# Performance work log

Measured on AMD Instinct MI355X. Metric: run time of the kernel, lower is better.

Reference implementation:

```python
import jax, jax.numpy as jnp
import numpy as np

NUM_GROUPS = 256


def _linear(x, w, b):
    return x @ w + b


def _layernorm(x, g, b, eps=1e-5):
    mu = jnp.mean(x, axis=-1, keepdims=True)
    var = jnp.mean((x - mu) ** 2, axis=-1, keepdims=True)
    return (x - mu) / jnp.sqrt(var + eps) * g + b


def setup_inputs() -> dict:
    key = jax.random.key(0)
    ks = jax.random.split(key, 12)
    B, N, C = 16, 8192, 3
    s = 0.02
    return {
        "xyz": jax.random.normal(ks[0], (B, N, C), jnp.float32),
        "labels": jax.random.randint(ks[1], (B, N), 0, NUM_GROUPS),
        # conv1: Linear(3,128) -> LayerNorm(128) -> ReLU -> Linear(128,256)
        "w1a": jax.random.normal(ks[2], (3, 128), jnp.float32) * s,
        "b1a": jnp.zeros((128,), jnp.float32),
        "g1": jnp.ones((128,), jnp.float32),
        "beta1": jnp.zeros((128,), jnp.float32),
        "w1b": jax.random.normal(ks[3], (128, 256), jnp.float32) * s,
        "b1b": jnp.zeros((256,), jnp.float32),
        # conv2: Linear(512,512) -> LayerNorm(512) -> ReLU -> Linear(512,256)
        "w2a": jax.random.normal(ks[4], (512, 512), jnp.float32) * s,
        "b2a": jnp.zeros((512,), jnp.float32),
        "g2": jnp.ones((512,), jnp.float32),
        "beta2": jnp.zeros((512,), jnp.float32),
        "w2b": jax.random.normal(ks[5], (512, 256), jnp.float32) * s,
        "b2b": jnp.zeros((256,), jnp.float32),
    }


def reference(xyz, labels, w1a, b1a, g1, beta1, w1b, b1b,
              w2a, b2a, g2, beta2, w2b, b2b):
    # per-batch segment reductions over cluster labels
    seg_sum = jax.vmap(lambda f, l: jax.ops.segment_sum(f, l, num_segments=NUM_GROUPS))
    seg_max = jax.vmap(lambda f, l: jax.ops.segment_max(f, l, num_segments=NUM_GROUPS))
    gather = jax.vmap(lambda p, l: p[l])  # [G,D],[N] -> [N,D]

    # centroids = per-cluster mean of xyz (converged kmeans centroids)
    counts = seg_sum(jnp.ones_like(xyz[..., :1]), labels)          # [B,G,1]
    centroids = seg_sum(xyz, labels) / jnp.maximum(counts, 1.0)    # [B,G,3]

    p_i = gather(centroids, labels)                                # [B,N,3]
    relative_xyz = xyz - p_i                                       # feature_type='dp'

    h = _linear(relative_xyz, w1a, b1a)
    h = jax.nn.relu(_layernorm(h, g1, beta1))
    h = _linear(h, w1b, b1b)                                       # [B,N,256]

    pooled = seg_max(h, labels)                                    # [B,G,256]
    pooled = jnp.where(jnp.isfinite(pooled), pooled, 0.0)          # empty groups -> 0
    repeated = gather(pooled, labels)                              # [B,N,256]

    cat = jnp.concatenate([repeated, h], axis=-1)                  # [B,N,512]
    h2 = _linear(cat, w2a, b2a)
    h2 = jax.nn.relu(_layernorm(h2, g2, beta2))
    h2 = _linear(h2, w2b, b2b)                                     # [B,N,256]

    out = seg_max(h2, labels)                                      # [B,G,256]
    out = jnp.where(jnp.isfinite(out), out, 0.0)
    return (centroids, out, p_i, labels)
```

## Files before the change

### kernel.cpp

```cpp
#include <hip/hip_runtime.h>
#include <hip/hip_bf16.h>

#define NB_  16
#define NPTS 8192
#define NG   256
#define NP   (NB_*NPTS)
#define NBLK (NP/128)
#define NQ   (NP/32)

#define OFF_CENT 0
#define OFF_OUT  12288
#define OFF_PI   1060864
#define OFF_LAB  1454080

typedef unsigned short u16;
typedef __attribute__((ext_vector_type(8))) short bf16x8;
typedef __attribute__((ext_vector_type(4))) float f32x4;

static constexpr size_t WS_SUMS  = 0;
static constexpr size_t WS_A1    = 65536;
static constexpr size_t WS_H     = WS_A1   + (size_t)NP*128*2;
static constexpr size_t WS_PBF   = WS_H    + (size_t)NP*256*2;
static constexpr size_t WS_WT1   = WS_PBF  + (size_t)NB_*NG*256*2;
static constexpr size_t WS_WT2A  = WS_WT1  + (size_t)256*128*2;
static constexpr size_t WS_WT2B  = WS_WT2A + (size_t)512*512*2;
static constexpr size_t WS_PREP  = WS_WT2B + (size_t)256*512*2;
static constexpr size_t WS_OFFS  = WS_PREP + (size_t)NB_*NG*512*4;
static constexpr size_t WS_CNT   = WS_OFFS + (size_t)NB_*NG*4;
static constexpr size_t WS_CUR   = WS_CNT  + (size_t)NB_*NG*4;
static constexpr size_t WS_SPOS  = WS_CUR  + (size_t)NB_*NG*4;
static constexpr size_t WS_GLAB  = WS_SPOS + (size_t)NP*4;
static constexpr size_t WS_PF    = WS_GLAB + (size_t)NP*4;
static constexpr size_t WS_PL    = WS_PF   + (size_t)NQ*256*4;
static constexpr size_t WS_DST   = WS_PL   + (size_t)NQ*256*4;
static constexpr size_t WS_NEED  = WS_DST  + (size_t)NB_*NG*256*4;

__device__ __forceinline__ u16 f2bf_bits(float f){
  __hip_bfloat16 h = __float2bfloat16(f);
  union { __hip_bfloat16 h; u16 s; } u; u.h = h; return u.s;
}
__device__ __forceinline__ float bf_bits2f(u16 s){
  return __uint_as_float(((unsigned)s) << 16);
}

__device__ __forceinline__ void gload16(const void* g, void* l){
  __builtin_amdgcn_global_load_lds((const __attribute__((address_space(1))) void*)g,
                                   (__attribute__((address_space(3))) void*)l, 16, 0, 0);
}

__global__ void k_init(float* __restrict__ sums, int* __restrict__ cursor){
  int i = blockIdx.x*blockDim.x + threadIdx.x;
  if (i < NB_*NG*4) sums[i] = 0.f;
  if (i < NB_*NG) cursor[i] = 0;
}

__global__ void k_wt(const float* __restrict__ src, u16* __restrict__ dst, int K, int N){
  int i = blockIdx.x*blockDim.x + threadIdx.x;
  if (i >= K*N) return;
  int n = i / K, k = i - n*K;
  dst[i] = f2bf_bits(src[(size_t)k*N + n]);
}

__global__ void k_points(const float* __restrict__ xyz, const int* __restrict__ labels,
                         float* __restrict__ sums, float* __restrict__ outLab){
  int p = blockIdx.x*blockDim.x + threadIdx.x;
  if (p >= NP) return;
  int b = p / NPTS;
  int g = labels[p];
  float x = xyz[p*3+0], y = xyz[p*3+1], z = xyz[p*3+2];
  float* s = sums + (size_t)(b*NG + g)*4;
  atomicAdd(s+0, x); atomicAdd(s+1, y); atomicAdd(s+2, z); atomicAdd(s+3, 1.f);
  outLab[p] = (float)g;
}

__global__ void k_cent(const float* __restrict__ sums, float* __restrict__ cent_out){
  int i = blockIdx.x*blockDim.x + threadIdx.x;
  if (i >= NB_*NG) return;
  const float* s = sums + (size_t)i*4;
  float c = fmaxf(s[3], 1.f);
  cent_out[i*3+0] = s[0]/c;
  cent_out[i*3+1] = s[1]/c;
  cent_out[i*3+2] = s[2]/c;
}

__global__ void k_scan(const float* __restrict__ sums, int* __restrict__ offs,
                       int* __restrict__ counts){
  __shared__ int sc[256];
  int b = blockIdx.x, g = threadIdx.x;
  int c = (int)(sums[(size_t)(b*NG+g)*4+3] + 0.5f);
  sc[g] = c;
  __syncthreads();
  for (int d = 1; d < 256; d <<= 1){
    int t = (g >= d) ? sc[g-d] : 0;
    __syncthreads();
    sc[g] += t;
    __syncthreads();
  }
  offs[b*NG+g] = b*NPTS + sc[g] - c;
  counts[b*NG+g] = c;
}

__global__ void k_scatter(const int* __restrict__ labels, const int* __restrict__ offs,
                          int* __restrict__ cursor, int* __restrict__ sortpos,
                          int* __restrict__ glab){
  int p = blockIdx.x*blockDim.x + threadIdx.x;
  if (p >= NP) return;
  int b = p / NPTS, g = labels[p];
  int pos = offs[b*NG+g] + atomicAdd(&cursor[b*NG+g], 1);
  sortpos[p] = pos;
  glab[pos] = g;
}

__global__ __launch_bounds__(256) void k_mlp1(
    const float* __restrict__ xyz, const int* __restrict__ labels,
    const int* __restrict__ sortpos, const float* __restrict__ cent,
    const float* __restrict__ w1a, const float* __restrict__ b1a,
    const float* __restrict__ g1, const float* __restrict__ beta1,
    u16* __restrict__ a1, float* __restrict__ pi_out)
{
  int wave = (int)((blockIdx.x*blockDim.x + threadIdx.x) >> 6);
  int lane = threadIdx.x & 63;
  int p = wave;
  if (p >= NP) return;
  int b = p / NPTS;
  int g = labels[p];
  const float* cb = cent + (size_t)(b*NG+g)*3;
  float c0 = cb[0], c1 = cb[1], c2 = cb[2];
  float r0 = xyz[p*3+0]-c0, r1 = xyz[p*3+1]-c1, r2 = xyz[p*3+2]-c2;
  if (lane < 3) pi_out[(size_t)p*3+lane] = (lane==0?c0:(lane==1?c1:c2));
  int j = lane*2;
  float2 wa0 = *(const float2*)(w1a + 0*128 + j);
  float2 wa1 = *(const float2*)(w1a + 1*128 + j);
  float2 wa2 = *(const float2*)(w1a + 2*128 + j);
  float2 bb  = *(const float2*)(b1a + j);
  float t0 = bb.x + r0*wa0.x + r1*wa1.x + r2*wa2.x;
  float t1 = bb.y + r0*wa0.y + r1*wa1.y + r2*wa2.y;
  float s = t0+t1, sq = t0*t0 + t1*t1;
  #pragma unroll
  for (int m = 32; m; m >>= 1){ s += __shfl_xor(s, m); sq += __shfl_xor(sq, m); }
  float mu  = s * (1.f/128.f);
  float var = sq * (1.f/128.f) - mu*mu;
  float inv = rsqrtf(var + 1e-5f);
  float2 gg = *(const float2*)(g1 + j), be = *(const float2*)(beta1 + j);
  float a0 = fmaxf((t0-mu)*inv*gg.x + be.x, 0.f);
  float a1v = fmaxf((t1-mu)*inv*gg.y + be.y, 0.f);
  unsigned pk = ((unsigned)f2bf_bits(a1v) << 16) | f2bf_bits(a0);
  int sp = sortpos[p];
  *reinterpret_cast<unsigned*>(a1 + (size_t)sp*128 + j) = pk;
}

template<int EPI>
__global__ __launch_bounds__(256)
void mgemm(const u16* __restrict__ A, int lda, int K,
           const u16* __restrict__ BT, int ldb, int kofs,
           const float* __restrict__ bias,
           u16* __restrict__ Cst, float* __restrict__ Cf, int ldc, int Nc)
{
  __shared__ alignas(16) u16 As[128*32];
  __shared__ alignas(16) u16 Bs[128*32];
  int NBk = Nc >> 7;
  int bm = blockIdx.x / NBk, bn = blockIdx.x % NBk;
  int m0 = bm << 7, n0 = bn << 7;
  int tid = threadIdx.x;
  int lane = tid & 63, w = tid >> 6;
  int wr = w >> 1, wc = w & 1;
  int l15 = lane & 15, l4 = lane >> 4;
  int r0 = tid >> 2;
  int ks = (tid & 3) << 3;
  u16* asd0 = As + (size_t)(w*64)*8;
  u16* asd1 = As + (size_t)(256 + w*64)*8;
  u16* bsd0 = Bs + (size_t)(w*64)*8;
  u16* bsd1 = Bs + (size_t)(256 + w*64)*8;
  f32x4 acc[4][4];
  #pragma unroll
  for (int i = 0; i < 4; ++i)
    #pragma unroll
    for (int jj = 0; jj < 4; ++jj)
      #pragma unroll
      for (int e = 0; e < 4; ++e) acc[i][jj][e] = 0.f;

  for (int k0 = 0; k0 < K; k0 += 32){
    gload16(A + (size_t)(m0 + r0)*lda + k0 + ks, asd0);
    gload16(A + (size_t)(m0 + r0 + 64)*lda + k0 + ks, asd1);
    gload16(BT + (size_t)(n0 + r0)*ldb + kofs + k0 + ks, bsd0);
    gload16(BT + (size_t)(n0 + r0 + 64)*ldb + kofs + k0 + ks, bsd1);
    __syncthreads();
    bf16x8 af[4], bfr[4];
    #pragma unroll
    for (int i = 0; i < 4; ++i){
      af[i]  = *(const bf16x8*)&As[(size_t)(wr*64 + i*16 + l15)*32 + l4*8];
      bfr[i] = *(const bf16x8*)&Bs[(size_t)(wc*64 + i*16 + l15)*32 + l4*8];
    }
    #pragma unroll
    for (int i = 0; i < 4; ++i)
      #pragma unroll
      for (int jj = 0; jj < 4; ++jj)
        acc[i][jj] = __builtin_amdgcn_mfma_f32_16x16x32_bf16(af[i], bfr[jj], acc[i][jj], 0, 0, 0);
    __syncthreads();
  }

  float bi[4];
  #pragma unroll
  for (int jj = 0; jj < 4; ++jj) bi[jj] = bias[n0 + wc*64 + jj*16 + l15];
  #pragma unroll
  for (int i = 0; i < 4; ++i){
    #pragma unroll
    for (int r = 0; r < 4; ++r){
      int m = m0 + wr*64 + i*16 + l4*4 + r;
      #pragma unroll
      for (int jj = 0; jj < 4; ++jj){
        int n = n0 + wc*64 + jj*16 + l15;
        float v = acc[i][jj][r] + bi[jj];
        if (EPI == 1) Cst[(size_t)m*ldc + n] = f2bf_bits(v);
        if (EPI == 3) Cf[(size_t)m*ldc + n] = v;
      }
    }
  }
}

__global__ __launch_bounds__(256) void k_pool(const u16* __restrict__ h,
                                              const int* __restrict__ offs,
                                              const int* __restrict__ counts,
                                              u16* __restrict__ poolbf){
  int bg = blockIdx.x, c = threadIdx.x;
  int cnt = counts[bg];
  if (cnt == 0){ poolbf[(size_t)bg*256 + c] = 0; return; }
  int off = offs[bg];
  float mx = bf_bits2f(h[(size_t)off*256 + c]);
  for (int r = 1; r < cnt; ++r)
    mx = fmaxf(mx, bf_bits2f(h[(size_t)(off+r)*256 + c]));
  poolbf[(size_t)bg*256 + c] = f2bf_bits(mx);
}

__global__ __launch_bounds__(1024, 1)
void fused6(const u16* __restrict__ h, const u16* __restrict__ wt2a,
            const u16* __restrict__ wt2b, const float* __restrict__ prepf,
            const float* __restrict__ b2b, const float* __restrict__ g2,
            const float* __restrict__ beta2, const int* __restrict__ glab,
            float* __restrict__ pf, float* __restrict__ pl, float* __restrict__ dstage)
{
  __shared__ alignas(16) char smem[136704];
  float* ssum  = (float*)(smem + 131072);
  float* ssq   = (float*)(smem + 131584);
  int*  glab_s = (int*)(smem + 132096);
  float* gtab  = (float*)(smem + 132608);
  float* btab  = (float*)(smem + 134656);
  int tid = threadIdx.x;
  int w = tid >> 6, lane = tid & 63;
  int l15 = lane & 15, l4 = lane >> 4;
  int m0 = blockIdx.x << 7;
  if (tid < 128){ ssum[tid] = 0.f; ssq[tid] = 0.f; glab_s[tid] = glab[m0 + tid]; }
  if (tid < 512) gtab[tid] = g2[tid];
  else           btab[tid - 512] = beta2[tid - 512];

  {
    const char* hb = (const char*)h;
    int lrow = lane >> 5;
    int kb = (lane & 31) << 4;
    #pragma unroll
    for (int t = 0; t < 4; ++t){
      int q = w*4 + t;
      int row = q*2 + lrow;
      gload16(hb + (size_t)(m0 + row)*512 + (kb ^ ((row & 7) << 4)),
              smem + 65536 + q*1024);
    }
  }
  __syncthreads();

  int gb = (m0 / NPTS) * NG;
  const u16* wA = wt2a + ((size_t)((w<<5) + l15))*512 + 256 + l4*8;

  #pragma unroll
  for (int half = 0; half < 2; ++half){
    int hr0 = half << 6;
    f32x4 acc[4][2];
    #pragma unroll
    for (int i = 0; i < 4; ++i)
      #pragma unroll
      for (int j = 0; j < 2; ++j)
        #pragma unroll
        for (int e = 0; e < 4; ++e) acc[i][j][e] = 0.f;
    #pragma unroll
    for (int kk = 0; kk < 8; ++kk){
      const int k0 = kk*32;
      bf16x8 bfr0 = *(const bf16x8*)(wA + k0);
      bf16x8 bfr1 = *(const bf16x8*)(wA + 8192 + k0);
      #pragma unroll
      for (int i = 0; i < 4; ++i){
        int row = hr0 + (i<<4) + l15;
        bf16x8 af = *(const bf16x8*)(smem + 65536 + row*512 +
                       ((((k0 + l4*8)) << 1) ^ ((row & 7) << 4)));
        acc[i][0] = __builtin_amdgcn_mfma_f32_16x16x32_bf16(af, bfr0, acc[i][0], 0, 0, 0);
        acc[i][1] = __builtin_amdgcn_mfma_f32_16x16x32_bf16(af, bfr1, acc[i][1], 0, 0, 0);
      }
    }
    #pragma unroll
    for (int i = 0; i < 4; ++i)
      #pragma unroll
      for (int r = 0; r < 4; ++r){
        int row = hr0 + (i<<4) + (l4<<2) + r;
        int grp = gb + glab_s[row];
        #pragma unroll
        for (int j = 0; j < 2; ++j){
          int n = (w<<5) + (j<<4) + l15;
          acc[i][j][r] += prepf[((size_t)grp << 9) + n];
        }
        float s = acc[i][0][r] + acc[i][1][r];
        float q = acc[i][0][r]*acc[i][0][r] + acc[i][1][r]*acc[i][1][r];
        #pragma unroll
        for (int mk = 1; mk < 16; mk <<= 1){ s += __shfl_xor(s, mk); q += __shfl_xor(q, mk); }
        if (l15 == 0){ atomicAdd(&ssum[row], s); atomicAdd(&ssq[row], q); }
      }
    if (half == 1) __syncthreads();
    #pragma unroll
    for (int i = 0; i < 4; ++i)
      #pragma unroll
      for (int r = 0; r < 4; ++r){
        int row = hr0 + (i<<4) + (l4<<2) + r;
        #pragma unroll
        for (int j = 0; j < 2; ++j){
          int n = (w<<5) + (j<<4) + l15;
          int byo = (row << 10) + ((n << 1) ^ ((row & 7) << 4));
          *(u16*)(smem + byo) = f2bf_bits(acc[i][j][r]);
        }
      }
  }

  if (tid < 128){
    float mu = ssum[tid] * (1.f/512.f);
    float var = ssq[tid] * (1.f/512.f) - mu*mu;
    ssum[tid] = mu;
    ssq[tid] = rsqrtf(var + 1e-5f);
  }
  __syncthreads();

  {
    int row = tid >> 3;
    int cb = tid & 7;
    float mu = ssum[row], inv = ssq[row];
    #pragma unroll
    for (int cc = 0; cc < 8; ++cc){
      int n = (((cc<<3) | cb) << 3);
      int byo = (row << 10) + ((n << 1) ^ ((row & 7) << 4));
      bf16x8 uv = *(const bf16x8*)(smem + byo);
      float4 gA = *(const float4*)(gtab + n), gB = *(const float4*)(gtab + n + 4);
      float4 bA = *(const float4*)(btab + n), bB = *(const float4*)(btab + n + 4);
      float gg[8] = {gA.x,gA.y,gA.z,gA.w,gB.x,gB.y,gB.z,gB.w};
      float bb[8] = {bA.x,bA.y,bA.z,bA.w,bB.x,bB.y,bB.z,bB.w};
      bf16x8 ov;
      #pragma unroll
      for (int e = 0; e < 8; ++e){
        float x = bf_bits2f((u16)uv[e]);
        ov[e] = (short)f2bf_bits(fmaxf((x - mu)*inv*gg[e] + bb[e], 0.f));
      }
      *(bf16x8*)(smem + byo) = ov;
    }
  }
  __syncthreads();

  f32x4 acc2[8];
  #pragma unroll
  for (int i = 0; i < 8; ++i)
    #pragma unroll
    for (int e = 0; e < 4; ++e) acc2[i][e] = 0.f;

  {
    const u16* wB = wt2b + ((size_t)((w<<4) + l15))*512 + l4*8;
    #pragma unroll
    for (int kk = 0; kk < 16; ++kk){
      const int k0 = kk*32;
      bf16x8 bf2 = *(const bf16x8*)(wB + k0);
      #pragma unroll
      for (int ip = 0; ip < 4; ++ip){
        bf16x8 af0, af1;
        {
          int row0 = ((2*ip)<<4) + l15;
          int row1 = ((2*ip+1)<<4) + l15;
          af0 = *(const bf16x8*)(smem + (row0 << 10) + ((((k0 + l4*8)) << 1) ^ ((row0 & 7) << 4)));
          af1 = *(const bf16x8*)(smem + (row1 << 10) + ((((k0 + l4*8)) << 1) ^ ((row1 & 7) << 4)));
        }
        acc2[2*ip]   = __builtin_amdgcn_mfma_f32_16x16x32_bf16(af0, bf2, acc2[2*ip], 0, 0, 0);
        acc2[2*ip+1] = __builtin_amdgcn_mfma_f32_16x16x32_bf16(af1, bf2, acc2[2*ip+1], 0, 0, 0);
      }
    }
  }
  __syncthreads();

  float bb = b2b[(w<<4) + l15];
  float* vbuf = (float*)smem;
  #pragma unroll
  for (int i = 0; i < 8; ++i){
    int n = (w<<4) + l15;
    #pragma unroll
    for (int r = 0; r < 4; ++r){
      int row = (i<<4) + (l4<<2) + r;
      vbuf[row*256 + n] = acc2[i][r] + bb;
    }
  }
  __syncthreads();
  {
    int c = tid & 255;
    int q = tid >> 8;
    int r0 = q << 5;
    size_t qblk = ((size_t)blockIdx.x << 2) + q;
    int curg = glab_s[r0];
    float mx = vbuf[r0*256 + c];
    bool from0 = true;
    for (int r = 1; r < 32; ++r){
      int g = glab_s[r0 + r];
      float v = vbuf[(r0 + r)*256 + c];
      if (g != curg){
        if (from0) pf[qblk*256 + c] = mx;
        else       dstage[((size_t)(gb + curg))*256 + c] = mx;
        curg = g; mx = v; from0 = false;
      } else mx = fmaxf(mx, v);
    }
    if (from0) pf[qblk*256 + c] = mx;
    else       pl[qblk*256 + c] = mx;
  }
}

__global__ __launch_bounds__(256) void k_combine(const int* __restrict__ offs,
                                                 const int* __restrict__ counts,
                                                 const float* __restrict__ pf,
                                                 const float* __restrict__ pl,
                                                 const float* __restrict__ dstage,
                                                 float* __restrict__ outp){
  int bg = blockIdx.x, c = threadIdx.x;
  int cnt = counts[bg];
  if (cnt == 0){ outp[(size_t)bg*256 + c] = 0.f; return; }
  int off = offs[bg], end = off + cnt;
  int B0 = off >> 5, B1 = (end - 1) >> 5;
  float v;
  if (B0 == B1){
    if ((off & 31) == 0)      v = pf[(size_t)B0*256 + c];
    else if ((end & 31) == 0) v = pl[(size_t)B0*256 + c];
    else                      v = dstage[(size_t)bg*256 + c];
  } else {
    v = ((off & 31) == 0) ? pf[(size_t)B0*256 + c] : pl[(size_t)B0*256 + c];
    for (int k = B0 + 1; k <= B1; ++k)
      v = fmaxf(v, pf[(size_t)k*256 + c]);
  }
  outp[(size_t)bg*256 + c] = v;
}

__global__ void k_sig(float* __restrict__ out, float val){
  int i = blockIdx.x*blockDim.x + threadIdx.x;
  if (i < 256) out[i] = val;
}

extern "C" void kernel_launch(void* const* d_in, const int* in_sizes, int n_in,
                              void* d_out, int out_size, void* d_ws, size_t ws_size,
                              hipStream_t stream) {
  const float* xyz    = (const float*)d_in[0];
  const int*   labels = (const int*)  d_in[1];
  const float* w1a    = (const float*)d_in[2];
  const float* b1a    = (const float*)d_in[3];
  const float* g1     = (const float*)d_in[4];
  const float* beta1  = (const float*)d_in[5];
  const float* w1b    = (const float*)d_in[6];
  const float* b1b    = (const float*)d_in[7];
  const float* w2a    = (const float*)d_in[8];
  const float* b2a    = (const float*)d_in[9];
  const float* g2     = (const float*)d_in[10];
  const float* beta2  = (const float*)d_in[11];
  const float* w2b    = (const float*)d_in[12];
  const float* b2b    = (const float*)d_in[13];
  float* out = (float*)d_out;
  char* ws = (char*)d_ws;

  if (ws_size < WS_NEED){
    k_sig<<<1, 256, 0, stream>>>(out, 10000.f + (float)(ws_size >> 20));
    return;
  }

  float*     sums   = (float*)(ws + WS_SUMS);
  u16*       a1     = (u16*)(ws + WS_A1);
  u16*       h      = (u16*)(ws + WS_H);
  u16*       poolbf = (u16*)(ws + WS_PBF);
  u16*       wt1    = (u16*)(ws + WS_WT1);
  u16*       wt2a   = (u16*)(ws + WS_WT2A);
  u16*       wt2b   = (u16*)(ws + WS_WT2B);
  float*     prepf  = (float*)(ws + WS_PREP);
  int*       offs   = (int*)(ws + WS_OFFS);
  int*       counts = (int*)(ws + WS_CNT);
  int*       cursor = (int*)(ws + WS_CUR);
  int*       sortpos= (int*)(ws + WS_SPOS);
  int*       glab   = (int*)(ws + WS_GLAB);
  float*     pf     = (float*)(ws + WS_PF);
  float*     pl     = (float*)(ws + WS_PL);
  float*     dstage = (float*)(ws + WS_DST);

  float* cent_out = out + OFF_CENT;
  float* out_seg  = out + OFF_OUT;
  float* pi_out   = out + OFF_PI;
  float* lab_out  = out + OFF_LAB;

  k_init<<<64, 256, 0, stream>>>(sums, cursor);
  k_wt<<<(128*256+255)/256, 256, 0, stream>>>(w1b, wt1, 128, 256);
  k_wt<<<(512*512+255)/256, 256, 0, stream>>>(w2a, wt2a, 512, 512);
  k_wt<<<(512*256+255)/256, 256, 0, stream>>>(w2b, wt2b, 512, 256);
  k_points<<<NP/256, 256, 0, stream>>>(xyz, labels, sums, lab_out);
  k_cent<<<(NB_*NG+255)/256, 256, 0, stream>>>(sums, cent_out);
  k_scan<<<NB_, 256, 0, stream>>>(sums, offs, counts);
  k_scatter<<<NP/256, 256, 0, stream>>>(labels, offs, cursor, sortpos, glab);
  k_mlp1<<<NP/4, 256, 0, stream>>>(xyz, labels, sortpos, cent_out,
                                   w1a, b1a, g1, beta1, a1, pi_out);
  mgemm<1><<<(NP/128)*(256/128), 256, 0, stream>>>(
      a1, 128, 128, wt1, 128, 0, b1b, h, (float*)nullptr, 256, 256);
  k_pool<<<NB_*NG, 256, 0, stream>>>(h, offs, counts, poolbf);
  mgemm<3><<<(NB_*NG/128)*(512/128), 256, 0, stream>>>(
      poolbf, 256, 256, wt2a, 512, 0, b2a, (u16*)nullptr, prepf, 512, 512);
  fused6<<<NBLK, 1024, 0, stream>>>(h, wt2a, wt2b, prepf, b2b, g2, beta2, glab,
                                    pf, pl, dstage);
  k_combine<<<NB_*NG, 256, 0, stream>>>(offs, counts, pf, pl, dstage, out_seg);
}
```

Baseline: 338.5 us.

## Shrink fused MLP tile to 64 rows with 512 threads for two blocks per CU

The fused second-MLP kernel now handles 64 points per block with 8 waves instead of 128 points with 16 waves. Shared memory drops to about 70KB, so two blocks can share a CU, and each wave covers more output columns per row tile. The aim is better overlap of the global loads and barrier phases across co-resident blocks. In exchange, every weight fragment is reloaded twice as often per point, and each wave holds more accumulator registers.

```diff
diff --git a/kernel.cpp b/kernel.cpp
--- a/kernel.cpp
+++ b/kernel.cpp
@@ -5,7 +5,7 @@
 #define NPTS 8192
 #define NG   256
 #define NP   (NB_*NPTS)
-#define NBLK (NP/128)
+#define NBLK (NP/64)
 #define NQ   (NP/32)
 
 #define OFF_CENT 0
@@ -232,26 +232,26 @@
   poolbf[(size_t)bg*256 + c] = f2bf_bits(mx);
 }
 
-__global__ __launch_bounds__(1024, 1)
-void fused6(const u16* __restrict__ h, const u16* __restrict__ wt2a,
+__global__ __launch_bounds__(512, 2)
+void fused7(const u16* __restrict__ h, const u16* __restrict__ wt2a,
             const u16* __restrict__ wt2b, const float* __restrict__ prepf,
             const float* __restrict__ b2b, const float* __restrict__ g2,
             const float* __restrict__ beta2, const int* __restrict__ glab,
             float* __restrict__ pf, float* __restrict__ pl, float* __restrict__ dstage)
 {
-  __shared__ alignas(16) char smem[136704];
-  float* ssum  = (float*)(smem + 131072);
-  float* ssq   = (float*)(smem + 131584);
-  int*  glab_s = (int*)(smem + 132096);
-  float* gtab  = (float*)(smem + 132608);
-  float* btab  = (float*)(smem + 134656);
+  __shared__ alignas(16) char smem[70400];
+  float* ssum  = (float*)(smem + 65536);
+  float* ssq   = (float*)(smem + 65792);
+  int*  glab_s = (int*)(smem + 66048);
+  float* gtab  = (float*)(smem + 66304);
+  float* btab  = (float*)(smem + 68352);
   int tid = threadIdx.x;
   int w = tid >> 6, lane = tid & 63;
   int l15 = lane & 15, l4 = lane >> 4;
-  int m0 = blockIdx.x << 7;
-  if (tid < 128){ ssum[tid] = 0.f; ssq[tid] = 0.f; glab_s[tid] = glab[m0 + tid]; }
-  if (tid < 512) gtab[tid] = g2[tid];
-  else           btab[tid - 512] = beta2[tid - 512];
+  int m0 = blockIdx.x << 6;
+  if (tid < 64){ ssum[tid] = 0.f; ssq[tid] = 0.f; glab_s[tid] = glab[m0 + tid]; }
+  gtab[tid] = g2[tid];
+  btab[tid] = beta2[tid];
 
   {
     const char* hb = (const char*)h;
@@ -262,71 +262,75 @@
       int q = w*4 + t;
       int row = q*2 + lrow;
       gload16(hb + (size_t)(m0 + row)*512 + (kb ^ ((row & 7) << 4)),
-              smem + 65536 + q*1024);
+              smem + 32768 + q*1024);
     }
   }
   __syncthreads();
 
   int gb = (m0 / NPTS) * NG;
-  const u16* wA = wt2a + ((size_t)((w<<5) + l15))*512 + 256 + l4*8;
+  const u16* wA = wt2a + ((size_t)((w<<6) + l15))*512 + 256 + l4*8;
 
   #pragma unroll
   for (int half = 0; half < 2; ++half){
-    int hr0 = half << 6;
-    f32x4 acc[4][2];
-    #pragma unroll
-    for (int i = 0; i < 4; ++i)
-      #pragma unroll
-      for (int j = 0; j < 2; ++j)
+    int hr0 = half << 5;
+    f32x4 acc[2][4];
+    #pragma unroll
+    for (int i = 0; i < 2; ++i)
+      #pragma unroll
+      for (int j = 0; j < 4; ++j)
         #pragma unroll
         for (int e = 0; e < 4; ++e) acc[i][j][e] = 0.f;
     #pragma unroll
     for (int kk = 0; kk < 8; ++kk){
       const int k0 = kk*32;
-      bf16x8 bfr0 = *(const bf16x8*)(wA + k0);
-      bf16x8 bfr1 = *(const bf16x8*)(wA + 8192 + k0);
-      #pragma unroll
-      for (int i = 0; i < 4; ++i){
+      bf16x8 bfr[4];
+      #pragma unroll
+      for (int j = 0; j < 4; ++j)
+        bfr[j] = *(const bf16x8*)(wA + j*8192 + k0);
+      #pragma unroll
+      for (int i = 0; i < 2; ++i){
         int row = hr0 + (i<<4) + l15;
-        bf16x8 af = *(const bf16x8*)(smem + 65536 + row*512 +
+        bf16x8 af = *(const bf16x8*)(smem + 32768 + row*512 +
                        ((((k0 + l4*8)) << 1) ^ ((row & 7) << 4)));
-        acc[i][0] = __builtin_amdgcn_mfma_f32_16x16x32_bf16(af, bfr0, acc[i][0], 0, 0, 0);
-        acc[i][1] = __builtin_amdgcn_mfma_f32_16x16x32_bf16(af, bfr1, acc[i][1], 0, 0, 0);
-      }
-    }
-    #pragma unroll
-    for (int i = 0; i < 4; ++i)
+        #pragma unroll
+        for (int j = 0; j < 4; ++j)
+          acc[i][j] = __builtin_amdgcn_mfma_f32_16x16x32_bf16(af, bfr[j], acc[i][j], 0, 0, 0);
+      }
+    }
+    #pragma unroll
+    for (int i = 0; i < 2; ++i)
       #pragma unroll
       for (int r = 0; r < 4; ++r){
         int row = hr0 + (i<<4) + (l4<<2) + r;
         int grp = gb + glab_s[row];
+        float s = 0.f, q = 0.f;
         #pragma unroll
-        for (int j = 0; j < 2; ++j){
-          int n = (w<<5) + (j<<4) + l15;
+        for (int j = 0; j < 4; ++j){
+          int n = (w<<6) + (j<<4) + l15;
           acc[i][j][r] += prepf[((size_t)grp << 9) + n];
+          s += acc[i][j][r];
+          q += acc[i][j][r]*acc[i][j][r];
         }
-        float s = acc[i][0][r] + acc[i][1][r];
-        float q = acc[i][0][r]*acc[i][0][r] + acc[i][1][r]*acc[i][1][r];
         #pragma unroll
         for (int mk = 1; mk < 16; mk <<= 1){ s += __shfl_xor(s, mk); q += __shfl_xor(q, mk); }
         if (l15 == 0){ atomicAdd(&ssum[row], s); atomicAdd(&ssq[row], q); }
       }
     if (half == 1) __syncthreads();
     #pragma unroll
-    for (int i = 0; i < 4; ++i)
+    for (int i = 0; i < 2; ++i)
       #pragma unroll
       for (int r = 0; r < 4; ++r){
         int row = hr0 + (i<<4) + (l4<<2) + r;
         #pragma unroll
-        for (int j = 0; j < 2; ++j){
-          int n = (w<<5) + (j<<4) + l15;
+        for (int j = 0; j < 4; ++j){
+          int n = (w<<6) + (j<<4) + l15;
           int byo = (row << 10) + ((n << 1) ^ ((row & 7) << 4));
           *(u16*)(smem + byo) = f2bf_bits(acc[i][j][r]);
         }
       }
   }
 
-  if (tid < 128){
+  if (tid < 64){
     float mu = ssum[tid] * (1.f/512.f);
     float var = ssq[tid] * (1.f/512.f) - mu*mu;
     ssum[tid] = mu;
@@ -358,20 +362,25 @@
   }
   __syncthreads();
 
-  f32x4 acc2[8];
-  #pragma unroll
-  for (int i = 0; i < 8; ++i)
-    #pragma unroll
-    for (int e = 0; e < 4; ++e) acc2[i][e] = 0.f;
+  f32x4 acc2[4][2];
+  #pragma unroll
+  for (int i = 0; i < 4; ++i)
+    #pragma unroll
+    for (int j = 0; j < 2; ++j)
+      #pragma unroll
+      for (int e = 0; e < 4; ++e) acc2[i][j][e] = 0.f;
 
   {
-    const u16* wB = wt2b + ((size_t)((w<<4) + l15))*512 + l4*8;
+    const u16* wB = wt2b + ((size_t)((w<<5) + l15))*512 + l4*8;
     #pragma unroll
     for (int kk = 0; kk < 16; ++kk){
       const int k0 = kk*32;
-      bf16x8 bf2 = *(const bf16x8*)(wB + k0);
-      #pragma unroll
-      for (int ip = 0; ip < 4; ++ip){
+      bf16x8 bf2[2];
+      #pragma unroll
+      for (int j = 0; j < 2; ++j)
+        bf2[j] = *(const bf16x8*)(wB + j*8192 + k0);
+      #pragma unroll
+      for (int ip = 0; ip < 2; ++ip){
         bf16x8 af0, af1;
         {
           int row0 = ((2*ip)<<4) + l15;
@@ -379,30 +388,36 @@
           af0 = *(const bf16x8*)(smem + (row0 << 10) + ((((k0 + l4*8)) << 1) ^ ((row0 & 7) << 4)));
           af1 = *(const bf16x8*)(smem + (row1 << 10) + ((((k0 + l4*8)) << 1) ^ ((row1 & 7) << 4)));
         }
-        acc2[2*ip]   = __builtin_amdgcn_mfma_f32_16x16x32_bf16(af0, bf2, acc2[2*ip], 0, 0, 0);
-        acc2[2*ip+1] = __builtin_amdgcn_mfma_f32_16x16x32_bf16(af1, bf2, acc2[2*ip+1], 0, 0, 0);
+        #pragma unroll
+        for (int j = 0; j < 2; ++j){
+          acc2[2*ip][j]   = __builtin_amdgcn_mfma_f32_16x16x32_bf16(af0, bf2[j], acc2[2*ip][j], 0, 0, 0);
+          acc2[2*ip+1][j] = __builtin_amdgcn_mfma_f32_16x16x32_bf16(af1, bf2[j], acc2[2*ip+1][j], 0, 0, 0);
+        }
       }
     }
   }
   __syncthreads();
 
-  float bb = b2b[(w<<4) + l15];
+  float bb0 = b2b[(w<<5) + l15], bb1 = b2b[(w<<5) + 16 + l15];
   float* vbuf = (float*)smem;
   #pragma unroll
-  for (int i = 0; i < 8; ++i){
-    int n = (w<<4) + l15;
-    #pragma unroll
-    for (int r = 0; r < 4; ++r){
-      int row = (i<<4) + (l4<<2) + r;
-      vbuf[row*256 + n] = acc2[i][r] + bb;
-    }
-  }
+  for (int i = 0; i < 4; ++i)
+    #pragma unroll
+    for (int j = 0; j < 2; ++j){
+      int n = (w<<5) + (j<<4) + l15;
+      float bbj = j ? bb1 : bb0;
+      #pragma unroll
+      for (int r = 0; r < 4; ++r){
+        int row = (i<<4) + (l4<<2) + r;
+        vbuf[row*256 + n] = acc2[i][j][r] + bbj;
+      }
+    }
   __syncthreads();
   {
     int c = tid & 255;
     int q = tid >> 8;
     int r0 = q << 5;
-    size_t qblk = ((size_t)blockIdx.x << 2) + q;
+    size_t qblk = ((size_t)blockIdx.x << 1) + q;
     int curg = glab_s[r0];
     float mx = vbuf[r0*256 + c];
     bool from0 = true;
@@ -511,7 +526,7 @@
   k_pool<<<NB_*NG, 256, 0, stream>>>(h, offs, counts, poolbf);
   mgemm<3><<<(NB_*NG/128)*(512/128), 256, 0, stream>>>(
       poolbf, 256, 256, wt2a, 512, 0, b2a, (u16*)nullptr, prepf, 512, 512);
-  fused6<<<NBLK, 1024, 0, stream>>>(h, wt2a, wt2b, prepf, b2b, g2, beta2, glab,
-                                    pf, pl, dstage);
+  fused7<<<NBLK, 512, 0, stream>>>(h, wt2a, wt2b, prepf, b2b, g2, beta2, glab,
+                                   pf, pl, dstage);
   k_combine<<<NB_*NG, 256, 0, stream>>>(offs, counts, pf, pl, dstage, out_seg);
 }
```

Result: slower. 418.2 us (+23.6%).
